# Optimization experiments

Measured on AMD Instinct MI355X. Metric: run time of the kernel, lower is better.

Reference implementation:

```python
import jax, jax.numpy as jnp
import numpy as np
from jax import lax

NQ, NS, D = 20000, 2000, 128
B, S = 32, 200
QN, CN = 4, 4
HOPS, RANK_K, MAXC = 3, 10, 4
NEG = -1e30


def setup_inputs() -> dict:
    key = jax.random.key(0)
    ks = jax.random.split(key, 40)
    n = lambda i, shape, s=0.05: jax.random.normal(ks[i], shape, jnp.float32) * s
    inp = {
        "question": jax.random.randint(ks[0], (B, S), 0, NQ),
        "response": jax.random.randint(ks[1], (B, S), 0, 2),
        "mask": jax.random.randint(ks[2], (B, S), 0, 2).astype(bool),
        "q_neighbors": jax.random.randint(ks[3], (NQ, QN), 0, NS),
        "s_neighbors": jax.random.randint(ks[4], (NS, CN), 0, NQ),
        "q_concept_idx": jax.random.randint(ks[5], (NQ, MAXC), 0, NS),
        "q_concept_mask": jax.random.randint(ks[6], (NQ, MAXC), 0, 2).astype(bool).at[:, 0].set(True),
        "embed_question": n(7, (NQ, D)),
        "embed_concept": n(8, (NS, D)),
        "embed_correctness": n(9, (2, D)),
        "gru1_wih": n(10, (3 * D, 2 * D)),
        "gru1_whh": n(11, (3 * D, D)),
        "gru1_bih": n(12, (3 * D,)),
        "gru1_bhh": n(13, (3 * D,)),
        "gru2_wih": n(14, (3 * D, D)),
        "gru2_whh": n(15, (3 * D, D)),
        "gru2_bih": n(16, (3 * D,)),
        "gru2_bhh": n(17, (3 * D,)),
        "agg_w": n(18, (HOPS, D, D)),
        "agg_b": n(19, (HOPS, D)),
        "agg_last_w": n(20, (D, D)),
        "agg_last_b": n(21, (D,)),
        "query_w": n(22, (D, D)),
        "query_b": n(23, (D,)),
        "key_w": n(24, (D, D)),
        "key_b": n(25, (D,)),
        "mlpW_w": n(26, (2 * D,)),
        "mlpW_b": n(27, (1,)),
        "h1_init": n(28, (B, D)),
        "h2_init": n(29, (B, D)),
    }
    return inp


def _gru(x, h, wih, whh, bih, bhh):
    # torch.nn.GRUCell math
    gi = x @ wih.T + bih
    gh = h @ whh.T + bhh
    ir, iz, inn = jnp.split(gi, 3, -1)
    hr, hz, hn = jnp.split(gh, 3, -1)
    r = jax.nn.sigmoid(ir + hr)
    z = jax.nn.sigmoid(iz + hz)
    return (1 - z) * jnp.tanh(inn + r * hn) + z * h


def _forward(question, response, mask, q_neighbors, s_neighbors, q_concept_idx,
             q_concept_mask, embed_question, embed_concept, embed_correctness,
             gru1_wih, gru1_whh, gru1_bih, gru1_bhh,
             gru2_wih, gru2_whh, gru2_bih, gru2_bhh,
             agg_w, agg_b, agg_last_w, agg_last_b,
             query_w, query_b, key_w, key_b, mlpW_w, mlpW_b,
             h1_init, h2_init):
    # ---- multi-hop GNN aggregation (dropout=eval). Computed for all B*S
    # positions and masked (equivalent to the masked-gather in the original). ----
    n0 = question.reshape(-1)            # [N]      question ids
    n1 = q_neighbors[n0]                 # [N,QN]   concept ids
    n2 = s_neighbors[n1]                 # [N,QN,CN] question ids
    n3 = q_neighbors[n2]                 # [N,QN,CN,QN] concept ids
    e = [embed_question[n0], embed_concept[n1], embed_question[n2], embed_concept[n3]]
    for i in range(HOPS):
        for j in range(HOPS - i):
            e[j] = jnp.tanh((e[j + 1].mean(-2) + e[j]) @ agg_w[j].T + agg_b[j])
    agg = jnp.tanh(e[0] @ agg_last_w.T + agg_last_b)
    emb_q_rec = jnp.where(mask.reshape(-1, 1), agg, embed_question[n0]).reshape(B, S, D)

    all_emb_q = embed_question[question]   # [B,S,D]
    emb_resp = embed_correctness[response]
    emb_c = embed_concept[q_concept_idx[question]] * q_concept_mask[question][..., None].astype(jnp.float32)
    # padded (masked-out) concept rows are zero -> contribute exactly 0 to the
    # attention-weighted sum, matching the original's dynamic slicing.
    qc_seq = jnp.concatenate([all_emb_q[:, 1:, None, :], emb_c[:, 1:]], axis=2)  # [B,S-1,1+MAXC,D]
    K_hist = lax.stop_gradient(all_emb_q)       # original detaches score inputs
    q_next = lax.stop_gradient(all_emb_q[:, 1:])
    w_q, w_k = mlpW_w[:D], mlpW_w[D:]
    pos = jnp.arange(S)

    def predict(qc, hist, hv):
        og = jnp.einsum('bqd,bsd->bqs', qc, hist)
        Kp = jnp.tanh(hist @ query_w.T + query_b)
        Qp = jnp.tanh(qc @ key_w.T + key_b)
        # MLP_W(concat(Q,K)) decomposes into two rank-1 terms
        tmp = (Qp @ w_q)[:, :, None] + (Kp @ w_k)[:, None, :] + mlpW_b[0]
        tmp = jnp.where(hv[:, None, :], tmp, NEG)
        alpha = jax.nn.softmax(tmp, axis=2)
        return jnp.sum(alpha * og, axis=(1, 2))

    def step(carry, xs):
        h1, h2, sh = carry
        t, er, eq, qc, qn = xs
        h1 = _gru(jnp.concatenate([eq, er], -1), h1, gru1_wih, gru1_whh, gru1_bih, gru1_bhh)
        g2 = _gru(h1, h2, gru2_wih, gru2_whh, gru2_bih, gru2_bhh)
        # top-k retrieval over history prefix 0..t-1 (masked); for t<=k the top-k
        # covers the entire valid prefix => identical math to taking all of it.
        sc = jnp.where(pos[None, :] < t, jnp.einsum('bsd,bd->bs', K_hist, qn), NEG)
        _, idx = lax.top_k(sc, RANK_K)
        sel = jnp.take_along_axis(sh, idx[:, :, None], axis=1)          # [B,k,D]
        hv = jnp.concatenate([jnp.ones((B, 1), bool), idx < t], axis=1)  # [B,k+1]
        hist = jnp.concatenate([g2[:, None], sel], axis=1)               # [B,k+1,D]
        p = predict(qc, hist, hv)
        # original skips h2/state_history update at t==0 (state_history[:,0] stays 0)
        keep = (t > 0).astype(g2.dtype)
        h2n = jnp.where(t == 0, h2, g2)
        sh = lax.dynamic_update_slice(sh, (g2 * keep)[:, None, :], (0, t, 0))
        return (h1, h2n, sh), p

    xs = (jnp.arange(S - 1),
          jnp.moveaxis(emb_resp[:, :S - 1], 1, 0),
          jnp.moveaxis(emb_q_rec[:, :S - 1], 1, 0),
          jnp.moveaxis(qc_seq, 1, 0),
          jnp.moveaxis(q_next, 1, 0))
    sh0 = jnp.zeros((B, S, D), jnp.float32)
    _, ys = lax.scan(step, (h1_init, h2_init, sh0), xs)  # ys: [S-1,B]
    y_hat = jnp.zeros((B, S), jnp.float32)
    y_hat = y_hat.at[:, 0].set(ys[0])
    y_hat = y_hat.at[:, 2:].set(ys[1:].T)  # y_hat[:,1] stays 0, as in original
    return y_hat


def reference(question, response, mask, q_neighbors, s_neighbors, q_concept_idx,
              q_concept_mask, embed_question, embed_concept, embed_correctness,
              gru1_wih, gru1_whh, gru1_bih, gru1_bhh,
              gru2_wih, gru2_whh, gru2_bih, gru2_bhh,
              agg_w, agg_b, agg_last_w, agg_last_b,
              query_w, query_b, key_w, key_b, mlpW_w, mlpW_b,
              h1_init, h2_init):
    return _forward(question, response, mask, q_neighbors, s_neighbors,
                    q_concept_idx, q_concept_mask, embed_question, embed_concept,
                    embed_correctness, gru1_wih, gru1_whh, gru1_bih, gru1_bhh,
                    gru2_wih, gru2_whh, gru2_bih, gru2_bhh, agg_w, agg_b,
                    agg_last_w, agg_last_b, query_w, query_b, key_w, key_b,
                    mlpW_w, mlpW_b, h1_init, h2_init)
```

## Files before the change

### kernel.cpp

```cpp
#include <hip/hip_runtime.h>
#include <math.h>

typedef unsigned short u16;
typedef unsigned int   u32;
typedef __attribute__((ext_vector_type(2))) _Float16 half2_t;

#define B_   32
#define S_   200
#define D_   128
#define T_   199
#define NEGV (-1e30f)

__device__ __forceinline__ float bf2f(u16 u){
  union { u32 i; float f; } v; v.i = ((u32)u) << 16; return v.f;
}
__device__ __forceinline__ u16 f2bf(float f){
  union { float f; u32 i; } v; v.f = f;
  u32 x = v.i;
  return (u16)((x + 0x7fffu + ((x >> 16) & 1u)) >> 16);
}
__device__ __forceinline__ u16 f2h(float x){
  union { _Float16 h; u16 u; } v; v.h = (_Float16)x; return v.u;
}
__device__ __forceinline__ float h2f(u16 u){
  union { u16 u; _Float16 h; } v; v.u = u; return (float)v.h;
}
__device__ __forceinline__ u32 pkh(float lo, float hi){
  return ((u32)f2h(hi) << 16) | f2h(lo);
}
__device__ __forceinline__ float dot2f(u32 w, u32 h, float acc){
#if __has_builtin(__builtin_amdgcn_fdot2)
  union { u32 u; half2_t h2; } a, b;
  a.u = w; b.u = h;
  return __builtin_amdgcn_fdot2(a.h2, b.h2, acc, false);
#else
  union { u32 u; _Float16 f[2]; } a, b;
  a.u = w; b.u = h;
  acc = fmaf((float)a.f[0], (float)b.f[0], acc);
  return fmaf((float)a.f[1], (float)b.f[1], acc);
#endif
}
__device__ __forceinline__ float fast_sigmoid(float x){ return 1.f/(1.f+__expf(-x)); }
__device__ __forceinline__ float fast_tanh(float x){
  float e = __expf(2.f*x);
  return 1.f - 2.f/(e + 1.f);
}

#define BARX() asm volatile("s_waitcnt lgkmcnt(0)\n\ts_barrier" ::: "memory")

#define PINV(x) asm volatile("" : "+v"(x))

__device__ __forceinline__ int readBool(const void* p, int i, int m){
  if (m == 0) return ((const int*)p)[i] != 0;
  if (m == 1) return ((const unsigned char*)p)[i] != 0;
  if (m == 2) return ((const u16*)p)[i] != 0;
  return ((const u32*)p)[i] != 0;
}

__device__ __forceinline__ float dot128f(const float* __restrict__ w,
                                         const float* __restrict__ x){
  float acc = 0.f;
  const float4* wp = (const float4*)w;
  #pragma unroll 8
  for (int i = 0; i < 32; i++){
    float4 v = wp[i]; int k = 4*i;
    acc = fmaf(v.x, x[k],   acc);
    acc = fmaf(v.y, x[k+1], acc);
    acc = fmaf(v.z, x[k+2], acc);
    acc = fmaf(v.w, x[k+3], acc);
  }
  return acc;
}

__global__ void k_sniff2(const u16* __restrict__ embq_raw,
                         const unsigned char* __restrict__ mask_raw,
                         int* __restrict__ flags){
  __shared__ int bad, gt1, m4, b0;
  const int tid = threadIdx.x;
  if (tid == 0){ bad = 0; gt1 = 0; m4 = 0; b0 = 0; }
  __syncthreads();
  for (int i = tid; i < 512; i += 256){
    u16 u = embq_raw[i];
    if (u){ int e = (u >> 7) & 0xFF; if (e < 0x58 || e > 0x7F) atomicAdd(&bad, 1); }
  }
  for (int i = tid; i < 1024; i += 256){
    unsigned char c = mask_raw[i];
    if (c > 1) atomicAdd(&gt1, 1);
    if (c && (i & 3)) atomicAdd(&m4, 1);
    if (c && !(i & 3)) atomicAdd(&b0, 1);
  }
  __syncthreads();
  if (tid == 0){
    flags[0] = (bad >= 16) ? 1 : 0;
    flags[1] = gt1 ? (b0 ? 2 : 3) : (m4 ? 1 : 0);
  }
}

#define NCVT 23
struct CvtArgs { const void* s[NCVT]; int off[NCVT+1]; int nreal[NCVT]; };

__global__ void k_cvt(CvtArgs a, const int* __restrict__ flags, float* __restrict__ dst){
  __shared__ int f;
  if (threadIdx.x == 0) f = flags[0];
  __syncthreads();
  int gid = blockIdx.x * 256 + threadIdx.x;
  if (gid >= a.off[NCVT]) return;
  int ai = 0;
  for (int i = 1; i < NCVT; i++) if (gid >= a.off[i]) ai = i;
  int i = gid - a.off[ai];
  float v = 0.f;
  if (i < a.nreal[ai])
    v = f ? ((const float*)a.s[ai])[i] : bf2f(((const u16*)a.s[ai])[i]);
  dst[gid] = v;
}

__global__ void k_prep(const float* __restrict__ WHH1, const float* __restrict__ WHH2,
                       const float* __restrict__ AW,   const float* __restrict__ ALW,
                       const float* __restrict__ WIH1, const float* __restrict__ WIH2,
                       const float* __restrict__ QW,
                       u16* __restrict__ WHH1h, u16* __restrict__ WHH2h,
                       u16* __restrict__ WIH2h,
                       u32* __restrict__ AWt,   u32* __restrict__ ALWt,
                       u32* __restrict__ WIH1t, float* __restrict__ QWt)
{
  const int gid0 = blockIdx.x*256 + threadIdx.x;
  const int stride = gridDim.x*256;
  for (int g = gid0; g < 49152; g += stride){
    WHH1h[g] = f2h(WHH1[g]);
    WHH2h[g] = f2h(WHH2[g]);
    WIH2h[g] = f2h(WIH2[g]);
  }
  for (int g = gid0; g < 24576; g += stride){
    int s = g >> 13, w = g & 8191;
    int k8 = w >> 9, r = w & 511, c = r >> 2, j = r & 3;
    const float* b = AW + s*16384 + c*128 + k8*8 + 2*j;
    AWt[g] = pkh(b[0], b[1]);
  }
  for (int g = gid0; g < 8192; g += stride){
    int k8 = g >> 9, r = g & 511, c = r >> 2, j = r & 3;
    const float* b = ALW + c*128 + k8*8 + 2*j;
    ALWt[g] = pkh(b[0], b[1]);
  }
  for (int g = gid0; g < 49152; g += stride){
    int k8 = g / 1536, r = g % 1536, c = r >> 2, j = r & 3;
    const float* b = WIH1 + c*256 + k8*8 + 2*j;
    WIH1t[g] = pkh(b[0], b[1]);
  }
  for (int g = gid0; g < 16384; g += stride){
    int k4 = g >> 9, r = g & 511, c = r >> 2, j = r & 3;
    QWt[g] = QW[c*128 + k4*4 + j];
  }
}

template<int ROWS>
__device__ __forceinline__ void agg_stage_h(const u16* __restrict__ tmph,
    const u32* __restrict__ Wt, const float* __restrict__ bg,
    u16* __restrict__ outh, int c)
{
  float bias = bg[c];
  float acc[ROWS];
  #pragma unroll
  for (int r = 0; r < ROWS; r++) acc[r] = bias;
  const uint4* wp = (const uint4*)Wt;
  if constexpr (ROWS <= 4){
    float acc2[ROWS];
    #pragma unroll
    for (int r = 0; r < ROWS; r++) acc2[r] = 0.f;
    #pragma unroll 4
    for (int g = 0; g < 16; g++){
      uint4 wv = wp[g*128 + c];
      #pragma unroll
      for (int r = 0; r < ROWS; r++){
        uint4 hv = *(const uint4*)(tmph + r*128 + g*8);
        acc[r]  = dot2f(wv.x, hv.x, acc[r]);
        acc2[r] = dot2f(wv.y, hv.y, acc2[r]);
        acc[r]  = dot2f(wv.z, hv.z, acc[r]);
        acc2[r] = dot2f(wv.w, hv.w, acc2[r]);
      }
    }
    #pragma unroll
    for (int r = 0; r < ROWS; r++)
      outh[r*128 + c] = f2h(fast_tanh(acc[r] + acc2[r]));
  } else {
    #pragma unroll 4
    for (int g = 0; g < 16; g++){
      uint4 wv = wp[g*128 + c];
      #pragma unroll
      for (int r = 0; r < ROWS; r++){
        uint4 hv = *(const uint4*)(tmph + r*128 + g*8);
        acc[r] = dot2f(wv.x, hv.x, acc[r]);
        acc[r] = dot2f(wv.y, hv.y, acc[r]);
        acc[r] = dot2f(wv.z, hv.z, acc[r]);
        acc[r] = dot2f(wv.w, hv.w, acc[r]);
      }
    }
    #pragma unroll
    for (int r = 0; r < ROWS; r++)
      outh[r*128 + c] = f2h(fast_tanh(acc[r]));
  }
}

__launch_bounds__(256, 4)
__global__ void k_agg(const int* __restrict__ question,
                      const int* __restrict__ q_neighbors,
                      const int* __restrict__ s_neighbors,
                      const float* __restrict__ EQ,
                      const float* __restrict__ EC,
                      const u32* __restrict__ AWt,
                      const float* __restrict__ AB,
                      const u32* __restrict__ ALWt,
                      const float* __restrict__ ALB,
                      const void* __restrict__ maskp,
                      const int* __restrict__ flags,
                      float* __restrict__ EQREC)
{
  __shared__ __align__(16) u16 e0h[2][128];
  __shared__ __align__(16) u16 e1h[2][512];
  __shared__ __align__(16) u16 e2h[2][2048];
  __shared__ __align__(16) u16 tmph[2][2048];
  __shared__ int nn1[2][4]; __shared__ int nn2[2][16]; __shared__ int nn3[2][64];
  __shared__ int mskS[2];
  const int tid  = threadIdx.x;
  const int c    = tid & 127;
  const int half = tid >> 7;
  const int bs   = blockIdx.x*2 + half;
  const int n0   = question[bs];
  u16* tp = tmph[half];

  if (c == 0) mskS[half] = readBool(maskp, bs, flags[1]);
  __syncthreads();
  const int msk = mskS[half];
  if ((mskS[0] | mskS[1]) == 0){
    EQREC[bs*128 + c] = EQ[n0*128 + c];
    return;
  }

  if (c < 4) nn1[half][c] = q_neighbors[n0*4 + c];
  __syncthreads();
  if (c < 16) nn2[half][c] = s_neighbors[nn1[half][c>>2]*4 + (c&3)];
  __syncthreads();
  if (c < 64) nn3[half][c] = q_neighbors[nn2[half][c>>2]*4 + (c&3)];
  e0h[half][c] = f2h(EQ[n0*128 + c]);
  #pragma unroll
  for (int r = 0; r < 4; r++)  e1h[half][r*128 + c] = f2h(EC[nn1[half][r]*128 + c]);
  #pragma unroll 4
  for (int r = 0; r < 16; r++) e2h[half][r*128 + c] = f2h(EQ[nn2[half][r]*128 + c]);
  __syncthreads();

  auto fill_e0 = [&](){
    float v = 0.25f*(h2f(e1h[half][c]) + h2f(e1h[half][128+c])
                   + h2f(e1h[half][256+c]) + h2f(e1h[half][384+c]))
            + h2f(e0h[half][c]);
    tp[c] = f2h(v);
  };
  auto fill_e1 = [&](){
    #pragma unroll
    for (int r = 0; r < 4; r++){
      float v = 0.25f*(h2f(e2h[half][(4*r)*128+c])   + h2f(e2h[half][(4*r+1)*128+c])
                     + h2f(e2h[half][(4*r+2)*128+c]) + h2f(e2h[half][(4*r+3)*128+c]))
              + h2f(e1h[half][r*128 + c]);
      tp[r*128 + c] = f2h(v);
    }
  };

  fill_e0(); __syncthreads();
  agg_stage_h<1>(tp, AWt, AB, e0h[half], c); __syncthreads();
  fill_e1(); __syncthreads();
  agg_stage_h<4>(tp, AWt + 8192, AB + 128, e1h[half], c); __syncthreads();
  #pragma unroll 2
  for (int r = 0; r < 16; r++){
    float m = 0.25f*( EC[nn3[half][4*r]*128+c]   + EC[nn3[half][4*r+1]*128+c]
                    + EC[nn3[half][4*r+2]*128+c] + EC[nn3[half][4*r+3]*128+c] );
    tp[r*128 + c] = f2h(m + h2f(e2h[half][r*128 + c]));
  }
  __syncthreads();
  agg_stage_h<16>(tp, AWt + 16384, AB + 256, e2h[half], c); __syncthreads();
  fill_e0(); __syncthreads();
  agg_stage_h<1>(tp, AWt, AB, e0h[half], c); __syncthreads();
  fill_e1(); __syncthreads();
  agg_stage_h<4>(tp, AWt + 8192, AB + 128, e1h[half], c); __syncthreads();
  fill_e0(); __syncthreads();
  agg_stage_h<1>(tp, AWt, AB, e0h[half], c); __syncthreads();
  agg_stage_h<1>(e0h[half], ALWt, ALB, tp, c); __syncthreads();
  EQREC[bs*128 + c] = msk ? h2f(tp[c]) : EQ[n0*128 + c];
}

__launch_bounds__(384, 1)
__global__ void k_gi1(const float* __restrict__ EQREC,
                      const int* __restrict__ response,
                      const float* __restrict__ ECOR,
                      const u32* __restrict__ WIH1t,
                      const float* __restrict__ BIH1,
                      float* __restrict__ GI1)
{
  const int t  = blockIdx.x;
  const int bg = blockIdx.y;
  const int tid = threadIdx.x;
  __shared__ __align__(16) u16 X[8][256];
  for (int o = tid; o < 2048; o += 384){
    int bb = o >> 8, k = o & 255;
    int b = bg*8 + bb;
    float v = (k < 128) ? EQREC[(b*S_ + t)*128 + k]
                        : ECOR[response[b*S_ + t]*128 + (k - 128)];
    X[bb][k] = f2h(v);
  }
  __syncthreads();
  float bias = BIH1[tid];
  float acc[8];
  #pragma unroll
  for (int i = 0; i < 8; i++) acc[i] = bias;
  const uint4* wp = (const uint4*)WIH1t;
  #pragma unroll 4
  for (int g = 0; g < 32; g++){
    uint4 wv = wp[g*384 + tid];
    #pragma unroll
    for (int bb = 0; bb < 8; bb++){
      uint4 hv = *(const uint4*)(&X[bb][g*8]);
      acc[bb] = dot2f(wv.x, hv.x, acc[bb]);
      acc[bb] = dot2f(wv.y, hv.y, acc[bb]);
      acc[bb] = dot2f(wv.z, hv.z, acc[bb]);
      acc[bb] = dot2f(wv.w, hv.w, acc[bb]);
    }
  }
  #pragma unroll
  for (int bb = 0; bb < 8; bb++)
    GI1[(t*32 + bg*8 + bb)*384 + tid] = acc[bb];
}

__global__ void k_topk(const int* __restrict__ question,
                       const float* __restrict__ EQ,
                       int* __restrict__ IDX)
{
  const int blk = blockIdx.x;
  const int t = blk >> 5, b = blk & 31;
  const int tid = threadIdx.x;
  __shared__ __align__(16) float qn[128];
  const int qid = question[b*S_ + t + 1];
  for (int o = tid; o < 128; o += 64) qn[o] = EQ[qid*128 + o];
  __syncthreads();
  float val[4]; int sv[4];
  #pragma unroll
  for (int i = 0; i < 4; i++){
    int s = tid + 64*i;
    sv[i] = s;
    float v = -3.0e38f;
    if (s < S_) v = (s < t) ? dot128f(EQ + question[b*S_ + s]*128, qn) : NEGV;
    val[i] = v;
  }
  for (int r = 0; r < 10; r++){
    float bv = -3.0e38f; int bi = 0x3fffffff;
    #pragma unroll
    for (int i = 0; i < 4; i++){
      if (val[i] > bv || (val[i] == bv && sv[i] < bi)){ bv = val[i]; bi = sv[i]; }
    }
    for (int off = 32; off; off >>= 1){
      float ov = __shfl_down(bv, off);
      int   oi = __shfl_down(bi, off);
      if (ov > bv || (ov == bv && oi < bi)){ bv = ov; bi = oi; }
    }
    int win = __shfl(bi, 0);
    if (tid == 0) IDX[blk*10 + r] = win;
    #pragma unroll
    for (int i = 0; i < 4; i++) if (sv[i] == win) val[i] = -3.0e38f;
  }
}

__launch_bounds__(768, 3)
__global__ void k_chain12(const float* __restrict__ GI1,
                          const u16* __restrict__ WHH1h, const float* __restrict__ BHH1,
                          const u16* __restrict__ WIH2h, const float* __restrict__ BIH2,
                          const u16* __restrict__ WHH2h, const float* __restrict__ BHH2,
                          const float* __restrict__ H1I, const float* __restrict__ H2I,
                          float* __restrict__ G2)
{
  const int b   = blockIdx.x;
  const int tid = threadIdx.x;
  __shared__ __align__(16) u16 hh1[128];
  __shared__ __align__(16) u16 hh2[128];
  __shared__ __align__(16) float psBuf[2304];

  int half, r0, sidx;
  const u16* wrow;
  const u16* hbase;
  float bias0, bias1, bias2;
  if (tid < 512){
    int i = tid;
    half = (i >= 256) ? 1 : 0; i -= half*256;
    r0 = 3*i;
    wrow  = ((r0 < 384) ? (WHH1h + r0*128) : (WIH2h + (r0-384)*128)) + half*64;
    hbase = hh1 + half*64;
    sidx  = half*768 + r0;
    if (half == 0){
      if (r0 < 384){ bias0 = BHH1[r0];     bias1 = BHH1[r0+1];   bias2 = BHH1[r0+2]; }
      else         { bias0 = BIH2[r0-384]; bias1 = BIH2[r0-383]; bias2 = BIH2[r0-382]; }
    } else { bias0 = bias1 = bias2 = 0.f; }
  } else {
    int j = tid - 512;
    half = (j >= 128) ? 1 : 0; j -= half*128;
    r0 = 3*j;
    wrow  = WHH2h + r0*128 + half*64;
    hbase = hh2 + half*64;
    sidx  = 1536 + half*384 + r0;
    if (half == 0){ bias0 = BHH2[r0]; bias1 = BHH2[r0+1]; bias2 = BHH2[r0+2]; }
    else { bias0 = bias1 = bias2 = 0.f; }
  }
  uint4 Wa[8], Wb[8], Wc[8];
  {
    const uint4* p0 = (const uint4*)(wrow);
    const uint4* p1 = (const uint4*)(wrow + 128);
    const uint4* p2 = (const uint4*)(wrow + 256);
    #pragma unroll
    for (int g = 0; g < 8; g++){ Wa[g] = p0[g]; Wb[g] = p1[g]; Wc[g] = p2[g]; }
  }
  #pragma unroll
  for (int g = 0; g < 8; g++){
    PINV(Wa[g].x); PINV(Wa[g].y); PINV(Wa[g].z); PINV(Wa[g].w);
    PINV(Wb[g].x); PINV(Wb[g].y); PINV(Wb[g].z); PINV(Wb[g].w);
    PINV(Wc[g].x); PINV(Wc[g].y); PINV(Wc[g].z); PINV(Wc[g].w);
  }

  auto mv = [&](){
    float a0 = bias0, a1 = bias1, a2 = bias2;
    #pragma unroll
    for (int g = 0; g < 8; g++){
      uint4 hv = *(const uint4*)(hbase + g*8);
      a0 = dot2f(Wa[g].x, hv.x, a0); a0 = dot2f(Wa[g].y, hv.y, a0);
      a0 = dot2f(Wa[g].z, hv.z, a0); a0 = dot2f(Wa[g].w, hv.w, a0);
      a1 = dot2f(Wb[g].x, hv.x, a1); a1 = dot2f(Wb[g].y, hv.y, a1);
      a1 = dot2f(Wb[g].z, hv.z, a1); a1 = dot2f(Wb[g].w, hv.w, a1);
      a2 = dot2f(Wc[g].x, hv.x, a2); a2 = dot2f(Wc[g].y, hv.y, a2);
      a2 = dot2f(Wc[g].z, hv.z, a2); a2 = dot2f(Wc[g].w, hv.w, a2);
    }
    psBuf[sidx] = a0; psBuf[sidx+1] = a1; psBuf[sidx+2] = a2;
  };

  float h1c = 0.f, h2c = 0.f;
  float pc0 = 0.f, pc1 = 0.f, pc2 = 0.f;
  if (tid < 128){
    h2c = H2I[b*128 + tid]; hh2[tid] = f2h(h2c);
  } else if (tid < 256){
    int u = tid - 128;
    h1c = H1I[b*128 + u]; hh1[u] = f2h(h1c);
    const float* gp = GI1 + b*384;
    pc0 = gp[u]; pc1 = gp[128+u]; pc2 = gp[256+u];
  }
  BARX();

  mv();
  BARX();
  if (tid >= 128 && tid < 256){
    int u = tid - 128;
    float r = fast_sigmoid(pc0 + psBuf[u]     + psBuf[768+u]);
    float z = fast_sigmoid(pc1 + psBuf[128+u] + psBuf[896+u]);
    float n = fast_tanh(pc2 + r*(psBuf[256+u] + psBuf[1024+u]));
    h1c = (1.f - z)*n + z*h1c;
    hh1[u] = f2h(h1c);
    const float* gp = GI1 + (32 + b)*384;
    pc0 = gp[u]; pc1 = gp[128+u]; pc2 = gp[256+u];
  }
  BARX();

  float* gout = G2 + b*128 + tid;
  #pragma unroll 1
  for (int t = 0; t < T_; t++){
    float pn0 = 0.f, pn1 = 0.f, pn2 = 0.f;
    if (tid >= 128 && tid < 256){
      int u = tid - 128;
      int tp = (t + 2 < T_) ? t + 2 : T_ - 1;
      const float* gp = GI1 + (tp*32 + b)*384;
      pn0 = gp[u]; pn1 = gp[128+u]; pn2 = gp[256+u];
    }
    mv();
    BARX();
    if (tid < 128){
      float cs0 = psBuf[384+tid]  + psBuf[1152+tid];
      float cs1 = psBuf[512+tid]  + psBuf[1280+tid];
      float cs2 = psBuf[640+tid]  + psBuf[1408+tid];
      float ds0 = psBuf[1536+tid] + psBuf[1920+tid];
      float ds1 = psBuf[1664+tid] + psBuf[2048+tid];
      float ds2 = psBuf[1792+tid] + psBuf[2176+tid];
      float r2 = fast_sigmoid(cs0 + ds0);
      float z2 = fast_sigmoid(cs1 + ds1);
      float n2 = fast_tanh(cs2 + r2*ds2);
      float g  = (1.f - z2)*n2 + z2*h2c;
      gout[t*4096] = g;
      if (t > 0) h2c = g;
      hh2[tid] = f2h(h2c);
    } else if (tid < 256){
      int u = tid - 128;
      float as0 = psBuf[u]     + psBuf[768+u];
      float as1 = psBuf[128+u] + psBuf[896+u];
      float as2 = psBuf[256+u] + psBuf[1024+u];
      float r1 = fast_sigmoid(pc0 + as0);
      float z1 = fast_sigmoid(pc1 + as1);
      float n1 = fast_tanh(pc2 + r1*as2);
      h1c = (1.f - z1)*n1 + z1*h1c;
      hh1[u] = f2h(h1c);
    }
    pc0 = pn0; pc1 = pn1; pc2 = pn2;
    BARX();
  }
}

__launch_bounds__(128, 4)
__global__ void k_kp(const float* __restrict__ G2,
                     const float* __restrict__ QWt, const float* __restrict__ QB,
                     const float* __restrict__ MW,
                     float* __restrict__ KPWG)
{
  __shared__ __align__(16) float X[8][128];
  __shared__ float red[8][2];
  const int tid = threadIdx.x;
  const int base = blockIdx.x * 8;
  for (int o = tid; o < 1024; o += 128){
    int r = o >> 7, c = o & 127;
    X[r][c] = G2[(base + r)*128 + c];
  }
  __syncthreads();
  float acc[8];
  float bias = QB[tid];
  #pragma unroll
  for (int r = 0; r < 8; r++) acc[r] = bias;
  const float4* wp = (const float4*)QWt;
  #pragma unroll 4
  for (int g = 0; g < 32; g++){
    float4 wv = wp[g*128 + tid];
    int kk = 4*g;
    #pragma unroll
    for (int r = 0; r < 8; r++){
      float4 t4 = *(const float4*)(&X[r][kk]);
      acc[r] = fmaf(t4.x, wv.x, acc[r]);
      acc[r] = fmaf(t4.y, wv.y, acc[r]);
      acc[r] = fmaf(t4.z, wv.z, acc[r]);
      acc[r] = fmaf(t4.w, wv.w, acc[r]);
    }
  }
  const float wk = MW[128 + tid];
  const int lane = tid & 63, wv_ = tid >> 6;
  #pragma unroll
  for (int r = 0; r < 8; r++){
    float pv = fast_tanh(acc[r]) * wk;
    for (int off = 32; off; off >>= 1) pv += __shfl_down(pv, off);
    if (lane == 0) red[r][wv_] = pv;
  }
  __syncthreads();
  if (tid < 8) KPWG[base + tid] = red[tid][0] + red[tid][1];
}

__global__ void k_pred(const int* __restrict__ question,
                       const int* __restrict__ qci, const void* __restrict__ qcm,
                       const int* __restrict__ flags,
                       const float* __restrict__ EQ, const float* __restrict__ EC,
                       const float* __restrict__ QB, const float* __restrict__ MW,
                       const float* __restrict__ G2,
                       const int* __restrict__ IDX,
                       const float* __restrict__ KPWG,
                       void* __restrict__ outp)
{
  const int blk = blockIdx.x;
  const int t = blk >> 5, b = blk & 31;
  const int tid = threadIdx.x;
  __shared__ float hist[11][132];
  __shared__ float qcs[128];
  __shared__ float og[11];
  __shared__ float kpw[11];
  __shared__ int   idxs[10];
  __shared__ float kpw0s;
  const int qid = question[b*S_ + t + 1];
  const int bflag = flags[1];
  if (tid < 10) idxs[tid] = IDX[blk*10 + tid];
  __syncthreads();
  for (int o = tid; o < 11*128; o += 64){
    int k = o >> 7, c = o & 127;
    float v;
    if (k == 0) v = G2[blk*128 + c];
    else { int s = idxs[k-1]; v = (s == 0) ? 0.f : G2[(s*32 + b)*128 + c]; }
    hist[k][c] = v;
  }
  #pragma unroll
  for (int o = tid; o < 128; o += 64){
    float v = EQ[qid*128 + o];
    #pragma unroll
    for (int q = 0; q < 4; q++){
      if (readBool(qcm, qid*4 + q, bflag))
        v += EC[qci[qid*4 + q]*128 + o];
    }
    qcs[o] = v;
  }
  {
    float pv = fast_tanh(QB[tid])      * MW[128 + tid]
             + fast_tanh(QB[tid + 64]) * MW[128 + tid + 64];
    for (int off = 32; off; off >>= 1) pv += __shfl_down(pv, off);
    if (tid == 0) kpw0s = pv;
  }
  __syncthreads();
  if (tid < 11){
    float acc = 0.f;
    for (int c = 0; c < 128; c++) acc = fmaf(qcs[c], hist[tid][c], acc);
    og[tid] = acc;
    float v;
    if (tid == 0) v = KPWG[blk];
    else { int s = idxs[tid-1]; v = (s == 0) ? kpw0s : KPWG[s*32 + b]; }
    kpw[tid] = v;
  }
  __syncthreads();
  if (tid == 0){
    float tv[11];
    #pragma unroll
    for (int k = 0; k < 11; k++){
      int valid = (k == 0) || (idxs[k-1] < t);
      tv[k] = valid ? kpw[k] : NEGV;
    }
    float m = tv[0];
    #pragma unroll
    for (int k = 1; k < 11; k++) m = fmaxf(m, tv[k]);
    float den = 0.f, num = 0.f;
    #pragma unroll
    for (int k = 0; k < 11; k++){
      float e = __expf(tv[k] - m);
      den += e;
      num = fmaf(e, og[k], num);
    }
    float p = num / den;
    int col = (t == 0) ? 0 : (t + 1);
    if (flags[0]){
      ((float*)outp)[b*S_ + col] = p;
      if (t == 0) ((float*)outp)[b*S_ + 1] = 0.f;
    } else {
      ((u16*)outp)[b*S_ + col] = f2bf(p);
      if (t == 0) ((u16*)outp)[b*S_ + 1] = (u16)0;
    }
  }
}

extern "C" void kernel_launch(void* const* d_in, const int* in_sizes, int n_in,
                              void* d_out, int out_size, void* d_ws, size_t ws_size,
                              hipStream_t stream)
{
  (void)in_sizes; (void)n_in; (void)out_size; (void)ws_size;
  const int* question      = (const int*)d_in[0];
  const int* response      = (const int*)d_in[1];
  const void* maskp        = d_in[2];
  const int* q_neighbors   = (const int*)d_in[3];
  const int* s_neighbors   = (const int*)d_in[4];
  const int* q_concept_idx = (const int*)d_in[5];
  const void* q_concept_mask = d_in[6];

  static const int CN[NCVT] = {2560000,256000,256,98304,49152,384,384,49152,49152,
                               384,384,49152,384,16384,128,16384,128,16384,128,
                               256,1,4096,4096};
  CvtArgs ca;
  int off = 0;
  for (int i = 0; i < NCVT; i++){
    ca.s[i] = d_in[7 + i];
    ca.nreal[i] = CN[i];
    ca.off[i] = off;
    off += (CN[i] + 3) & ~3;
  }
  ca.off[NCVT] = off;
  const int total = off;

  char* ws = (char*)d_ws;
  size_t wo = 0;
  auto alloc = [&](size_t bytes) -> void* {
    void* p = ws + wo;
    wo = (wo + bytes + 255) & ~(size_t)255;
    return p;
  };
  int*   flags = (int*)  alloc(16);
  float* CVT   = (float*)alloc((size_t)total * 4);
  float* EQREC = (float*)alloc((size_t)B_*S_*D_*4);
  float* GI1   = (float*)alloc((size_t)T_*B_*384*4);
  float* G2    = (float*)alloc((size_t)T_*B_*D_*4);
  int*   IDX   = (int*)  alloc((size_t)T_*B_*10*4);
  float* KPWG  = (float*)alloc((size_t)T_*B_*4);
  u16*   WHH1h = (u16*)  alloc(49152*2);
  u16*   WHH2h = (u16*)  alloc(49152*2);
  u16*   WIH2h = (u16*)  alloc(49152*2);
  u32*   AWt   = (u32*)  alloc(24576*4);
  u32*   ALWt  = (u32*)  alloc(8192*4);
  u32*   WIH1t = (u32*)  alloc(49152*4);
  float* QWt   = (float*)alloc(16384*4);

  const float* EQ   = CVT + ca.off[0];
  const float* EC   = CVT + ca.off[1];
  const float* ECOR = CVT + ca.off[2];
  const float* WIH1 = CVT + ca.off[3];
  const float* WHH1 = CVT + ca.off[4];
  const float* BIH1 = CVT + ca.off[5];
  const float* BHH1 = CVT + ca.off[6];
  const float* WIH2 = CVT + ca.off[7];
  const float* WHH2 = CVT + ca.off[8];
  const float* BIH2 = CVT + ca.off[9];
  const float* BHH2 = CVT + ca.off[10];
  const float* AW   = CVT + ca.off[11];
  const float* AB   = CVT + ca.off[12];
  const float* ALW  = CVT + ca.off[13];
  const float* ALB  = CVT + ca.off[14];
  const float* QW   = CVT + ca.off[15];
  const float* QB   = CVT + ca.off[16];
  const float* MW   = CVT + ca.off[19];
  const float* H1I  = CVT + ca.off[21];
  const float* H2I  = CVT + ca.off[22];

  k_sniff2<<<1, 256, 0, stream>>>((const u16*)d_in[7], (const unsigned char*)maskp, flags);
  k_cvt<<<(total + 255)/256, 256, 0, stream>>>(ca, flags, CVT);
  k_prep<<<192, 256, 0, stream>>>(WHH1, WHH2, AW, ALW, WIH1, WIH2, QW,
                                  WHH1h, WHH2h, WIH2h, AWt, ALWt, WIH1t, QWt);
  k_agg<<<B_*S_/2, 256, 0, stream>>>(question, q_neighbors, s_neighbors, EQ, EC,
                                     AWt, AB, ALWt, ALB, maskp, flags, EQREC);
  k_gi1<<<dim3(T_, 4), 384, 0, stream>>>(EQREC, response, ECOR, WIH1t, BIH1, GI1);
  k_topk<<<T_*B_, 64, 0, stream>>>(question, EQ, IDX);
  k_chain12<<<B_, 768, 0, stream>>>(GI1, WHH1h, BHH1, WIH2h, BIH2, WHH2h, BHH2,
                                    H1I, H2I, G2);
  k_kp<<<T_*B_/8, 128, 0, stream>>>(G2, QWt, QB, MW, KPWG);
  k_pred<<<T_*B_, 64, 0, stream>>>(question, q_concept_idx, q_concept_mask, flags,
                                   EQ, EC, QB, MW, G2, IDX, KPWG, d_out);
}
```

Baseline: 531.8 us.

## Fold top-k selection into the GRU chain kernel to overlap it with the recurrence

Removes the separate top-k kernel and runs its work in extra blocks of the sequential GRU chain kernel, one wave per (t,b) pair. The 32 chain blocks get raised scheduling priority. The aim is to hide the top-k cost behind the latency-bound recurrence, which only occupies 32 blocks. The risks are extra LDS use per block, which may reduce occupancy, and top-k blocks competing with the chain blocks for CU resources.

```diff
diff --git a/kernel.cpp b/kernel.cpp
--- a/kernel.cpp
+++ b/kernel.cpp
@@ -327,57 +327,63 @@
     GI1[(t*32 + bg*8 + bb)*384 + tid] = acc[bb];
 }
 
-__global__ void k_topk(const int* __restrict__ question,
-                       const float* __restrict__ EQ,
-                       int* __restrict__ IDX)
-{
-  const int blk = blockIdx.x;
-  const int t = blk >> 5, b = blk & 31;
-  const int tid = threadIdx.x;
-  __shared__ __align__(16) float qn[128];
-  const int qid = question[b*S_ + t + 1];
-  for (int o = tid; o < 128; o += 64) qn[o] = EQ[qid*128 + o];
-  __syncthreads();
-  float val[4]; int sv[4];
-  #pragma unroll
-  for (int i = 0; i < 4; i++){
-    int s = tid + 64*i;
-    sv[i] = s;
-    float v = -3.0e38f;
-    if (s < S_) v = (s < t) ? dot128f(EQ + question[b*S_ + s]*128, qn) : NEGV;
-    val[i] = v;
-  }
-  for (int r = 0; r < 10; r++){
-    float bv = -3.0e38f; int bi = 0x3fffffff;
-    #pragma unroll
-    for (int i = 0; i < 4; i++){
-      if (val[i] > bv || (val[i] == bv && sv[i] < bi)){ bv = val[i]; bi = sv[i]; }
-    }
-    for (int off = 32; off; off >>= 1){
-      float ov = __shfl_down(bv, off);
-      int   oi = __shfl_down(bi, off);
-      if (ov > bv || (ov == bv && oi < bi)){ bv = ov; bi = oi; }
-    }
-    int win = __shfl(bi, 0);
-    if (tid == 0) IDX[blk*10 + r] = win;
-    #pragma unroll
-    for (int i = 0; i < 4; i++) if (sv[i] == win) val[i] = -3.0e38f;
-  }
-}
-
 __launch_bounds__(768, 3)
 __global__ void k_chain12(const float* __restrict__ GI1,
                           const u16* __restrict__ WHH1h, const float* __restrict__ BHH1,
                           const u16* __restrict__ WIH2h, const float* __restrict__ BIH2,
                           const u16* __restrict__ WHH2h, const float* __restrict__ BHH2,
                           const float* __restrict__ H1I, const float* __restrict__ H2I,
-                          float* __restrict__ G2)
+                          float* __restrict__ G2,
+                          const int* __restrict__ question,
+                          const float* __restrict__ EQ,
+                          int* __restrict__ IDX)
 {
-  const int b   = blockIdx.x;
   const int tid = threadIdx.x;
   __shared__ __align__(16) u16 hh1[128];
   __shared__ __align__(16) u16 hh2[128];
   __shared__ __align__(16) float psBuf[2304];
+  __shared__ __align__(16) float qns[12][128];
+
+  if (blockIdx.x >= 32){
+    const int wv = tid >> 6, lane = tid & 63;
+    const int p = (blockIdx.x - 32)*12 + wv;
+    if (p >= T_*B_) return;
+    const int t = p >> 5, bq = p & 31;
+    const int qid = question[bq*S_ + t + 1];
+    float* qn = qns[wv];
+    qn[lane]      = EQ[qid*128 + lane];
+    qn[lane + 64] = EQ[qid*128 + 64 + lane];
+    asm volatile("s_waitcnt lgkmcnt(0)" ::: "memory");
+    float val[4]; int sv[4];
+    #pragma unroll
+    for (int i = 0; i < 4; i++){
+      int s = lane + 64*i;
+      sv[i] = s;
+      float v = -3.0e38f;
+      if (s < S_) v = (s < t) ? dot128f(EQ + question[bq*S_ + s]*128, qn) : NEGV;
+      val[i] = v;
+    }
+    for (int r = 0; r < 10; r++){
+      float bv = -3.0e38f; int bi = 0x3fffffff;
+      #pragma unroll
+      for (int i = 0; i < 4; i++){
+        if (val[i] > bv || (val[i] == bv && sv[i] < bi)){ bv = val[i]; bi = sv[i]; }
+      }
+      for (int off = 32; off; off >>= 1){
+        float ov = __shfl_down(bv, off);
+        int   oi = __shfl_down(bi, off);
+        if (ov > bv || (ov == bv && oi < bi)){ bv = ov; bi = oi; }
+      }
+      int win = __shfl(bi, 0);
+      if (lane == 0) IDX[p*10 + r] = win;
+      #pragma unroll
+      for (int i = 0; i < 4; i++) if (sv[i] == win) val[i] = -3.0e38f;
+    }
+    return;
+  }
+
+  __builtin_amdgcn_s_setprio(1);
+  const int b = blockIdx.x;
 
   int half, r0, sidx;
   const u16* wrow;
@@ -703,6 +709,8 @@
   const float* H1I  = CVT + ca.off[21];
   const float* H2I  = CVT + ca.off[22];
 
+  const int TOPK_BLOCKS = (T_*B_ + 11) / 12;
+
   k_sniff2<<<1, 256, 0, stream>>>((const u16*)d_in[7], (const unsigned char*)maskp, flags);
   k_cvt<<<(total + 255)/256, 256, 0, stream>>>(ca, flags, CVT);
   k_prep<<<192, 256, 0, stream>>>(WHH1, WHH2, AW, ALW, WIH1, WIH2, QW,
@@ -710,9 +718,9 @@
   k_agg<<<B_*S_/2, 256, 0, stream>>>(question, q_neighbors, s_neighbors, EQ, EC,
                                      AWt, AB, ALWt, ALB, maskp, flags, EQREC);
   k_gi1<<<dim3(T_, 4), 384, 0, stream>>>(EQREC, response, ECOR, WIH1t, BIH1, GI1);
-  k_topk<<<T_*B_, 64, 0, stream>>>(question, EQ, IDX);
-  k_chain12<<<B_, 768, 0, stream>>>(GI1, WHH1h, BHH1, WIH2h, BIH2, WHH2h, BHH2,
-                                    H1I, H2I, G2);
+  k_chain12<<<32 + TOPK_BLOCKS, 768, 0, stream>>>(GI1, WHH1h, BHH1, WIH2h, BIH2,
+                                                  WHH2h, BHH2, H1I, H2I, G2,
+                                                  question, EQ, IDX);
   k_kp<<<T_*B_/8, 128, 0, stream>>>(G2, QWt, QB, MW, KPWG);
   k_pred<<<T_*B_, 64, 0, stream>>>(question, q_concept_idx, q_concept_mask, flags,
                                    EQ, EC, QB, MW, G2, IDX, KPWG, d_out);
```

Result: faster. 473.8 us, median of 2 (-10.9%).
